# Performance work log

Measured on AMD Instinct MI355X. Metric: run time of the kernel, lower is better.

The kernel has to match this reference:

```python
import jax, jax.numpy as jnp
import numpy as np
import math

DIM, DEPTH, HEADS, DH, MLP = 512, 12, 8, 64, 2048
EPS = 1e-5

def _ln(x, g, b):
    m = jnp.mean(x, -1, keepdims=True)
    v = jnp.var(x, -1, keepdims=True)
    return (x - m) * jax.lax.rsqrt(v + EPS) * g + b

def _gelu(x):
    return jax.nn.gelu(x, approximate=False)  # torch nn.GELU default = exact erf

def _conv1d(x, w, b):
    # x: [B, Cin, T], w: [Cout, Cin, 7], 'same' padding
    y = jax.lax.conv_general_dilated(x, w, (1,), [(3, 3)], dimension_numbers=('NCH', 'OIH', 'NCH'))
    return y + b[None, :, None]

def setup_inputs() -> dict:
    key = jax.random.key(0)
    ks = iter(jax.random.split(key, 64))
    def w(shape, s=0.02):
        return jax.random.normal(next(ks), shape, jnp.float32) * s
    return {
        'x': jax.random.normal(next(ks), (2, 1024), jnp.float32),
        'timesteps': jax.random.uniform(next(ks), (2,), jnp.float32) * 1000.0,
        'cond': jax.random.normal(next(ks), (2, 64, DIM), jnp.float32),
        'conv_w1': w((DIM // 2, 1, 7)), 'conv_b1': jnp.zeros((DIM // 2,), jnp.float32),
        'conv_w2': w((DIM, DIM // 2, 7)), 'conv_b2': jnp.zeros((DIM,), jnp.float32),
        'tpe_w1': w((DIM, 4 * DIM)), 'tpe_b1': jnp.zeros((4 * DIM,), jnp.float32),
        'tpe_w2': w((4 * DIM, DIM)), 'tpe_b2': jnp.zeros((DIM,), jnp.float32),
        'ln1_g': jnp.ones((DEPTH, DIM), jnp.float32), 'ln1_b': jnp.zeros((DEPTH, DIM), jnp.float32),
        'wq': w((DEPTH, DIM, HEADS * DH)), 'wkv': w((DEPTH, DIM, 2 * DH)),
        'wo': w((DEPTH, HEADS * DH, DIM)), 'bo': jnp.zeros((DEPTH, DIM), jnp.float32),
        'ln2_g': jnp.ones((DEPTH, DIM), jnp.float32), 'ln2_b': jnp.zeros((DEPTH, DIM), jnp.float32),
        'ffn_w1': w((DEPTH, DIM, MLP)), 'ffn_b1': jnp.zeros((DEPTH, MLP), jnp.float32),
        'ffn_w2': w((DEPTH, MLP, DIM)), 'ffn_b2': jnp.zeros((DEPTH, DIM), jnp.float32),
        'tm_w1': w((DEPTH, DIM, 4 * DIM)), 'tm_b1': jnp.zeros((DEPTH, 4 * DIM), jnp.float32),
        'tm_w2': w((DEPTH, 4 * DIM, DIM)), 'tm_b2': jnp.zeros((DEPTH, DIM), jnp.float32),
        'fn_g': jnp.ones((DIM,), jnp.float32), 'fn_b': jnp.zeros((DIM,), jnp.float32),
        'out_w1': w((DIM, 2 * DIM)), 'out_b1': jnp.zeros((2 * DIM,), jnp.float32),
        'out_w2': w((2 * DIM, 1)), 'out_b2': jnp.zeros((1,), jnp.float32),
    }

def reference(x, timesteps, cond, conv_w1, conv_b1, conv_w2, conv_b2,
              tpe_w1, tpe_b1, tpe_w2, tpe_b2,
              ln1_g, ln1_b, wq, wkv, wo, bo, ln2_g, ln2_b,
              ffn_w1, ffn_b1, ffn_w2, ffn_b2, tm_w1, tm_b1, tm_w2, tm_b2,
              fn_g, fn_b, out_w1, out_b1, out_w2, out_b2):
    b, T = x.shape
    # audio encoder: conv -> relu -> conv -> relu
    h = _conv1d(x[:, None, :], conv_w1, conv_b1)
    h = jax.nn.relu(h)
    h = _conv1d(h, conv_w2, conv_b2)
    h = jax.nn.relu(h)
    h = h.transpose(0, 2, 1)  # [b, T, dim]
    # sinusoidal time embedding + MLP
    half = DIM // 2
    freqs = jnp.exp(jnp.arange(half, dtype=jnp.float32) * (-math.log(10000.0) / (half - 1)))
    te = timesteps[:, None] * freqs[None, :]
    te = jnp.concatenate([jnp.sin(te), jnp.cos(te)], axis=-1)  # [b, dim]
    time_emb = _gelu(te @ tpe_w1 + tpe_b1) @ tpe_w2 + tpe_b2
    # concat text conditioning tokens
    h = jnp.concatenate([h, cond], axis=1)  # [b, n, dim]
    bsz, n, _ = h.shape
    scale = DH ** -0.5

    def block(hx, p):
        g1, b1, Wq, Wkv, Wo, Bo, g2, b2, F1, Fb1, F2, Fb2, T1, Tb1, T2, Tb2 = p
        tm = _gelu(time_emb @ T1 + Tb1) @ T2 + Tb2  # [b, dim]
        hx = _ln(hx, g1, b1)
        q = (hx @ Wq).reshape(bsz, n, HEADS, DH).transpose(0, 2, 1, 3)  # [b,h,n,d]
        kv = hx @ Wkv
        k, v = kv[..., :DH], kv[..., DH:]  # shared single KV head [b,n,d]
        dots = jnp.einsum('bhnd,bmd->bhnm', q, k) * scale
        attn = jax.nn.softmax(dots, axis=-1)
        o = jnp.einsum('bhnm,bmd->bhnd', attn, v)
        o = o.transpose(0, 2, 1, 3).reshape(bsz, n, HEADS * DH) @ Wo + Bo
        hx = hx + o
        hx = hx + tm[:, None, :]
        hx = _ln(hx, g2, b2)
        hx = hx + (_gelu(hx @ F1 + Fb1) @ F2 + Fb2)
        return hx, None

    h, _ = jax.lax.scan(block, h, (ln1_g, ln1_b, wq, wkv, wo, bo, ln2_g, ln2_b,
                                   ffn_w1, ffn_b1, ffn_w2, ffn_b2,
                                   tm_w1, tm_b1, tm_w2, tm_b2))
    h = _ln(h, fn_g, fn_b)
    h = _gelu(h @ out_w1 + out_b1) @ out_w2 + out_b2  # [b, n, 1]
    return h[:, :T, 0]
```

## Files before the change

### kernel.cpp

```cpp
#include <hip/hip_runtime.h>
#include <hip/hip_bf16.h>
#include <math.h>


typedef unsigned short u16;
typedef __attribute__((ext_vector_type(8))) short short8;
typedef __attribute__((ext_vector_type(8))) unsigned short ushort8;
typedef __attribute__((ext_vector_type(4))) float f32x4;

#define MFMA_B16(a, b, c) __builtin_amdgcn_mfma_f32_16x16x32_bf16(a, b, c, 0, 0, 0)

__device__ __forceinline__ float gelu_f(float x) {
  return 0.5f * x * (1.f + erff(x * 0.70710678118654752f));
}
__device__ __forceinline__ u16 f2b(float x) {
  union { float f; unsigned u; } v;
  v.f = x;
  unsigned r = (v.u + 0x7FFF + ((v.u >> 16) & 1)) >> 16;
  return (u16)r;
}
__device__ __forceinline__ float b2f(u16 u) {
  union { unsigned u; float f; } v;
  v.u = ((unsigned)u) << 16;
  return v.f;
}

#define MODE_BIAS 1
#define MODE_GELU 2
#define MODE_RES 4
#define MODE_TM 8
#define MODE_OUT16 16
#define MODE_KVT 32
#define MODE_RELU 64
#define MODE_CONVROW 128

__global__ void te_k(const float* __restrict__ ts, float* __restrict__ te) {
  int t = threadIdx.x;
  int b = t >> 8, i = t & 255;
  float tv = ts[b];
  float fr = __expf((float)i * (-9.210340371976184f / 255.f));
  float arg = tv * fr;
  te[b * 512 + i] = sinf(arg);
  te[b * 512 + 256 + i] = cosf(arg);
}

__global__ __launch_bounds__(256) void mlpA_k(const float* __restrict__ A,
                                              const float* __restrict__ B,
                                              float* __restrict__ part, int K,
                                              int N, long sA, long sB) {
  int l = blockIdx.z;
  const float* Ap = A + (size_t)l * sA;
  const float* Bp = B + (size_t)l * sB;
  int KS = K >> 7;
  int tid = threadIdx.x;
  int c16 = tid & 15;
  int col = blockIdx.x * 64 + c16 * 4;
  int kr = tid >> 4;
  int k0 = blockIdx.y * 128 + kr;
  float4 a0 = {0.f, 0.f, 0.f, 0.f}, a1 = {0.f, 0.f, 0.f, 0.f};
#pragma unroll
  for (int i = 0; i < 8; ++i) {
    int k = k0 + i * 16;
    float4 bv = *(const float4*)&Bp[(size_t)k * N + col];
    float x0 = Ap[k], x1 = Ap[K + k];
    a0.x = fmaf(x0, bv.x, a0.x);
    a0.y = fmaf(x0, bv.y, a0.y);
    a0.z = fmaf(x0, bv.z, a0.z);
    a0.w = fmaf(x0, bv.w, a0.w);
    a1.x = fmaf(x1, bv.x, a1.x);
    a1.y = fmaf(x1, bv.y, a1.y);
    a1.z = fmaf(x1, bv.z, a1.z);
    a1.w = fmaf(x1, bv.w, a1.w);
  }
#pragma unroll
  for (int off = 16; off < 64; off <<= 1) {
    a0.x += __shfl_xor(a0.x, off);
    a0.y += __shfl_xor(a0.y, off);
    a0.z += __shfl_xor(a0.z, off);
    a0.w += __shfl_xor(a0.w, off);
    a1.x += __shfl_xor(a1.x, off);
    a1.y += __shfl_xor(a1.y, off);
    a1.z += __shfl_xor(a1.z, off);
    a1.w += __shfl_xor(a1.w, off);
  }
  __shared__ float red[4][2][64];
  int w = tid >> 6, lane = tid & 63;
  if (lane < 16) {
    *(float4*)&red[w][0][c16 * 4] = a0;
    *(float4*)&red[w][1][c16 * 4] = a1;
  }
  __syncthreads();
  if (tid < 128) {
    int m = tid >> 6, c = tid & 63;
    float s = red[0][m][c] + red[1][m][c] + red[2][m][c] + red[3][m][c];
    part[(((size_t)l * KS + blockIdx.y) * 2 + m) * N + blockIdx.x * 64 + c] = s;
  }
}

__global__ __launch_bounds__(256) void mlpB_k(const float* __restrict__ part,
                                              const float* __restrict__ bias,
                                              float* __restrict__ C, int N,
                                              int lgN, int KS, int dogelu,
                                              long sb, long sC) {
  int idx = blockIdx.x * 256 + threadIdx.x;
  int col = idx & (N - 1);
  int lm = idx >> lgN;
  int m = lm & 1, l = lm >> 1;
  float s = 0.f;
  for (int ks = 0; ks < KS; ++ks)
    s += part[(((size_t)l * KS + ks) * 2 + m) * N + col];
  s += bias[(size_t)l * sb + col];
  if (dogelu) s = gelu_f(s);
  C[(size_t)l * sC + (size_t)m * N + col] = s;
}

__global__ __launch_bounds__(256) void conv1_k(const float* __restrict__ x,
                                               const float* __restrict__ w1,
                                               const float* __restrict__ b1,
                                               float* __restrict__ buf1) {
  int idx = blockIdx.x * 256 + threadIdx.x;
  int t = idx & 1023, co = (idx >> 10) & 255, b = idx >> 18;
  float acc = b1[co];
#pragma unroll
  for (int k = 0; k < 7; ++k) {
    int gt = t + k - 3;
    if (gt >= 0 && gt < 1024)
      acc = fmaf(w1[co * 7 + k], x[b * 1024 + gt], acc);
  }
  buf1[idx] = fmaxf(acc, 0.f);
}

__global__ __launch_bounds__(256) void im2col_k(const float* __restrict__ buf1,
                                                u16* __restrict__ A16) {
  int idx = blockIdx.x * 256 + threadIdx.x;
  int c = idx % 1792;
  int m = idx / 1792;
  int b = m >> 10, tt = m & 1023;
  int ci = c / 7, k = c - ci * 7;
  int gt = tt + k - 3;
  float v = (gt >= 0 && gt < 1024) ? buf1[((b * 256) + ci) * 1024 + gt] : 0.f;
  A16[idx] = f2b(v);
}

__global__ void cond_k(const float* __restrict__ cond,
                       float* __restrict__ hbuf) {
  int idx = blockIdx.x * 256 + threadIdx.x;
  int b = idx >> 15, rem = idx & 32767;
  int j = rem >> 9, cc = rem & 511;
  hbuf[(size_t)(b * 1088 + 1024 + j) * 512 + cc] = cond[idx];
}

__global__ __launch_bounds__(256) void ln_k(float* __restrict__ h,
                                            u16* __restrict__ h16,
                                            const float* __restrict__ g,
                                            const float* __restrict__ bb) {
  int row = blockIdx.x;
  float* p = h + (size_t)row * 512;
  int t = threadIdx.x;
  float x0 = p[t], x1 = p[t + 256];
  float s = x0 + x1, q = x0 * x0 + x1 * x1;
#pragma unroll
  for (int off = 1; off < 64; off <<= 1) {
    s += __shfl_xor(s, off);
    q += __shfl_xor(q, off);
  }
  __shared__ float ps[4], pq[4];
  int w = t >> 6, lane = t & 63;
  if (lane == 0) {
    ps[w] = s;
    pq[w] = q;
  }
  __syncthreads();
  s = ps[0] + ps[1] + ps[2] + ps[3];
  q = pq[0] + pq[1] + pq[2] + pq[3];
  float mean = s * (1.f / 512.f);
  float var = q * (1.f / 512.f) - mean * mean;
  float rs = rsqrtf(var + 1e-5f);
  float v0 = (x0 - mean) * rs * g[t] + bb[t];
  float v1 = (x1 - mean) * rs * g[t + 256] + bb[t + 256];
  p[t] = v0;
  p[t + 256] = v1;
  h16[(size_t)row * 512 + t] = f2b(v0);
  h16[(size_t)row * 512 + t + 256] = f2b(v1);
}

__device__ __forceinline__ void wcvt_tile(float (*T)[65],
                                          const float* __restrict__ src,
                                          u16* __restrict__ dst, int K, int N,
                                          int tk, int tn, int t) {
  int kl = t >> 2, nseg = (t & 3) * 16;
#pragma unroll
  for (int j = 0; j < 4; ++j) {
    float4 v =
        *(const float4*)&src[(size_t)(tk * 64 + kl) * N + tn * 64 + nseg + j * 4];
    T[nseg + j * 4 + 0][kl] = v.x;
    T[nseg + j * 4 + 1][kl] = v.y;
    T[nseg + j * 4 + 2][kl] = v.z;
    T[nseg + j * 4 + 3][kl] = v.w;
  }
  __syncthreads();
  int nl = t >> 2, kseg = (t & 3) * 16;
#pragma unroll
  for (int j = 0; j < 4; ++j) {
    ushort4 o;
    o.x = f2b(T[nl][kseg + j * 4 + 0]);
    o.y = f2b(T[nl][kseg + j * 4 + 1]);
    o.z = f2b(T[nl][kseg + j * 4 + 2]);
    o.w = f2b(T[nl][kseg + j * 4 + 3]);
    *(ushort4*)&dst[(size_t)(tn * 64 + nl) * K + tk * 64 + kseg + j * 4] = o;
  }
}

__global__ __launch_bounds__(256) void wcvt5_k(
    const float* wq, const float* wkv, const float* wo, const float* w1,
    const float* w2, u16* dq, u16* dkv, u16* dwo, u16* d1, u16* d2) {
  __shared__ float T[64][65];
  int bid = blockIdx.x, t = threadIdx.x;
  if (bid < 64) {
    wcvt_tile(T, wq, dq, 512, 512, bid >> 3, bid & 7, t);
  } else if (bid < 80) {
    int id = bid - 64;
    wcvt_tile(T, wkv, dkv, 512, 128, id >> 1, id & 1, t);
  } else if (bid < 144) {
    int id = bid - 80;
    wcvt_tile(T, wo, dwo, 512, 512, id >> 3, id & 7, t);
  } else if (bid < 400) {
    int id = bid - 144;
    wcvt_tile(T, w1, d1, 512, 2048, id >> 5, id & 31, t);
  } else {
    int id = bid - 400;
    wcvt_tile(T, w2, d2, 2048, 512, id >> 3, id & 7, t);
  }
}

__global__ __launch_bounds__(256) void wcvtT_k(const float* src, u16* dst,
                                               int K, int N) {
  __shared__ float T[64][65];
  int nt = N >> 6;
  int tk = blockIdx.x / nt, tn = blockIdx.x % nt;
  wcvt_tile(T, src, dst, K, N, tk, tn, threadIdx.x);
}

__global__ __launch_bounds__(256) void fcvt_k(const float* __restrict__ src,
                                              u16* __restrict__ dst, int n) {
  int i = (blockIdx.x * 256 + threadIdx.x) * 4;
  if (i >= n) return;
  float4 v = *(const float4*)&src[i];
  ushort4 o;
  o.x = f2b(v.x);
  o.y = f2b(v.y);
  o.z = f2b(v.z);
  o.w = f2b(v.w);
  *(ushort4*)&dst[i] = o;
}

__global__ __launch_bounds__(256) void bgemm2_k(
    const u16* __restrict__ A, const u16* __restrict__ B,
    const float* __restrict__ bias, const float* __restrict__ tmv,
    const float* __restrict__ res, float* __restrict__ Cf,
    u16* __restrict__ C16, u16* __restrict__ C16b, float* __restrict__ part,
    int K, int N, int Kblk, int MN, int mode) {
  __shared__ u16 As[2][64 * 72];
  __shared__ u16 Bs[2][64 * 72];
  int t = threadIdx.x;
  int n0 = blockIdx.x * 64, m0 = blockIdx.y * 64;
  int kz = blockIdx.z;
  int wid = t >> 6, lane = t & 63;
  int quad = lane >> 4, l15 = lane & 15;
  int wr = (wid >> 1) * 32, wc = (wid & 1) * 32;
  int sr = t >> 2, sc = (t & 3) * 16;
  const u16* Ap = A + (size_t)(m0 + sr) * K + (size_t)kz * Kblk + sc;
  const u16* Bp = B + (size_t)(n0 + sr) * K + (size_t)kz * Kblk + sc;

  f32x4 acc[2][2];
#pragma unroll
  for (int i = 0; i < 2; ++i)
#pragma unroll
    for (int j = 0; j < 2; ++j) acc[i][j] = (f32x4){0.f, 0.f, 0.f, 0.f};

  int nt = Kblk >> 6;
  ushort8 ra0 = *(const ushort8*)Ap;
  ushort8 ra1 = *(const ushort8*)(Ap + 8);
  ushort8 rb0 = *(const ushort8*)Bp;
  ushort8 rb1 = *(const ushort8*)(Bp + 8);
  *(ushort8*)&As[0][sr * 72 + sc] = ra0;
  *(ushort8*)&As[0][sr * 72 + sc + 8] = ra1;
  *(ushort8*)&Bs[0][sr * 72 + sc] = rb0;
  *(ushort8*)&Bs[0][sr * 72 + sc + 8] = rb1;
  __syncthreads();
  int cur = 0;
  for (int tt = 0; tt < nt; ++tt) {
    if (tt + 1 < nt) {
      const u16* ap = Ap + (tt + 1) * 64;
      const u16* bp = Bp + (tt + 1) * 64;
      ra0 = *(const ushort8*)ap;
      ra1 = *(const ushort8*)(ap + 8);
      rb0 = *(const ushort8*)bp;
      rb1 = *(const ushort8*)(bp + 8);
    }
    short8 af[2][2], bf[2][2];
#pragma unroll
    for (int s = 0; s < 2; ++s)
#pragma unroll
      for (int i = 0; i < 2; ++i) {
        af[i][s] =
            *(const short8*)&As[cur][(wr + i * 16 + l15) * 72 + s * 32 + quad * 8];
        bf[i][s] =
            *(const short8*)&Bs[cur][(wc + i * 16 + l15) * 72 + s * 32 + quad * 8];
      }
#pragma unroll
    for (int s = 0; s < 2; ++s)
#pragma unroll
      for (int i = 0; i < 2; ++i)
#pragma unroll
        for (int j = 0; j < 2; ++j)
          acc[i][j] = MFMA_B16(af[i][s], bf[j][s], acc[i][j]);
    if (tt + 1 < nt) {
      int nx = cur ^ 1;
      *(ushort8*)&As[nx][sr * 72 + sc] = ra0;
      *(ushort8*)&As[nx][sr * 72 + sc + 8] = ra1;
      *(ushort8*)&Bs[nx][sr * 72 + sc] = rb0;
      *(ushort8*)&Bs[nx][sr * 72 + sc + 8] = rb1;
      __syncthreads();
      cur = nx;
    }
  }

  if (gridDim.z > 1) {
#pragma unroll
    for (int i = 0; i < 2; ++i)
#pragma unroll
      for (int reg = 0; reg < 4; ++reg) {
        int row = m0 + wr + i * 16 + quad * 4 + reg;
#pragma unroll
        for (int j = 0; j < 2; ++j) {
          int col = n0 + wc + j * 16 + l15;
          part[(size_t)kz * MN + (size_t)row * N + col] = acc[i][j][reg];
        }
      }
    return;
  }

#pragma unroll
  for (int i = 0; i < 2; ++i) {
#pragma unroll
    for (int reg = 0; reg < 4; ++reg) {
      int row = m0 + wr + i * 16 + quad * 4 + reg;
      int orow = (mode & MODE_CONVROW) ? row + ((row >> 10) << 6) : row;
#pragma unroll
      for (int j = 0; j < 2; ++j) {
        int col = n0 + wc + j * 16 + l15;
        float v = acc[i][j][reg];
        if (mode & MODE_BIAS) v += bias[col];
        if (mode & MODE_TM) v += tmv[(row >= 1088 ? 512 : 0) + col];
        if (mode & MODE_RES) v += res[(size_t)orow * 512 + col];
        if (mode & MODE_GELU) v = gelu_f(v);
        if (mode & MODE_RELU) v = fmaxf(v, 0.f);
        if (mode & MODE_KVT) {
          if (col < 64)
            C16[orow * 64 + col] = f2b(v);
          else
            C16b[(size_t)(col - 64) * 2176 + orow] = f2b(v);
        } else if (mode & MODE_OUT16) {
          C16[(size_t)orow * N + col] = f2b(v);
        } else {
          Cf[(size_t)orow * N + col] = v;
        }
      }
    }
  }
}

__global__ __launch_bounds__(256) void bred_k(
    const float* __restrict__ part, const float* __restrict__ bias,
    const float* __restrict__ tmv, const float* __restrict__ res,
    float* __restrict__ Cf, u16* __restrict__ C16, u16* __restrict__ C16b,
    int MN, int Nmask, int lgN, int S, int mode) {
  int idx = (blockIdx.x * 256 + threadIdx.x) * 4;
  if (idx >= MN) return;
  int row = idx >> lgN;
  int col = idx & Nmask;
  float4 s = *(const float4*)&part[idx];
  for (int ss = 1; ss < S; ++ss) {
    float4 p = *(const float4*)&part[(size_t)ss * MN + idx];
    s.x += p.x;
    s.y += p.y;
    s.z += p.z;
    s.w += p.w;
  }
  float v[4] = {s.x, s.y, s.z, s.w};
#pragma unroll
  for (int j = 0; j < 4; ++j) {
    float vv = v[j];
    int c = col + j;
    if (mode & MODE_BIAS) vv += bias[c];
    if (mode & MODE_TM) vv += tmv[(row >= 1088 ? 512 : 0) + c];
    if (mode & MODE_RES) vv += res[(size_t)row * 512 + c];
    if (mode & MODE_GELU) vv = gelu_f(vv);
    v[j] = vv;
  }
  if (mode & MODE_KVT) {
    if (col < 64) {
      ushort4 o;
      o.x = f2b(v[0]);
      o.y = f2b(v[1]);
      o.z = f2b(v[2]);
      o.w = f2b(v[3]);
      *(ushort4*)&C16[row * 64 + col] = o;
    } else {
#pragma unroll
      for (int j = 0; j < 4; ++j)
        C16b[(size_t)(col - 64 + j) * 2176 + row] = f2b(v[j]);
    }
  } else if (mode & MODE_OUT16) {
    ushort4 o;
    o.x = f2b(v[0]);
    o.y = f2b(v[1]);
    o.z = f2b(v[2]);
    o.w = f2b(v[3]);
    *(ushort4*)&C16[idx] = o;
  } else {
    float4 o = {v[0], v[1], v[2], v[3]};
    *(float4*)&Cf[idx] = o;
  }
}

__global__ __launch_bounds__(256) void attn_k(const u16* __restrict__ q,
                                              const u16* __restrict__ k16,
                                              const u16* __restrict__ vT16,
                                              u16* __restrict__ o) {
  __shared__ u16 Qs[64 * 72];
  __shared__ u16 Ks[64 * 72];
  __shared__ u16 VT[64 * 72];
  __shared__ u16 Ps[64 * 72];
  int t = threadIdx.x;
  int qt = blockIdx.x, h = blockIdx.y, b = blockIdx.z;
  int wid = t >> 6, lane = t & 63;
  int quad = lane >> 4, l15 = lane & 15;
  int w16 = wid * 16;
  {
    int r = t >> 2, seg = (t & 3) * 16;
    const u16* qp = q + (size_t)(b * 1088 + qt * 64 + r) * 512 + h * 64 + seg;
    *(ushort8*)&Qs[r * 72 + seg] = *(const ushort8*)qp;
    *(ushort8*)&Qs[r * 72 + seg + 8] = *(const ushort8*)(qp + 8);
  }
  f32x4 accO[4];
#pragma unroll
  for (int i = 0; i < 4; ++i) accO[i] = (f32x4){0.f, 0.f, 0.f, 0.f};
  float mi[4] = {-1e30f, -1e30f, -1e30f, -1e30f};
  float li[4] = {0.f, 0.f, 0.f, 0.f};

  for (int kt = 0; kt < 17; ++kt) {
    __syncthreads();
    {
      int r = t >> 2, seg = (t & 3) * 16;
      const u16* kp = k16 + (size_t)(b * 1088 + kt * 64 + r) * 64 + seg;
      *(ushort8*)&Ks[r * 72 + seg] = *(const ushort8*)kp;
      *(ushort8*)&Ks[r * 72 + seg + 8] = *(const ushort8*)(kp + 8);
      const u16* vp = vT16 + (size_t)r * 2176 + b * 1088 + kt * 64 + seg;
      *(ushort8*)&VT[r * 72 + seg] = *(const ushort8*)vp;
      *(ushort8*)&VT[r * 72 + seg + 8] = *(const ushort8*)(vp + 8);
    }
    __syncthreads();
    f32x4 sc[4];
#pragma unroll
    for (int sn = 0; sn < 4; ++sn) sc[sn] = (f32x4){0.f, 0.f, 0.f, 0.f};
#pragma unroll
    for (int s = 0; s < 2; ++s) {
      short8 a = *(const short8*)&Qs[(w16 + l15) * 72 + s * 32 + quad * 8];
#pragma unroll
      for (int sn = 0; sn < 4; ++sn) {
        short8 bb = *(const short8*)&Ks[(sn * 16 + l15) * 72 + s * 32 + quad * 8];
        sc[sn] = MFMA_B16(a, bb, sc[sn]);
      }
    }
#pragma unroll
    for (int reg = 0; reg < 4; ++reg) {
      float s0 = sc[0][reg] * 0.125f, s1 = sc[1][reg] * 0.125f;
      float s2 = sc[2][reg] * 0.125f, s3 = sc[3][reg] * 0.125f;
      float mx = fmaxf(fmaxf(s0, s1), fmaxf(s2, s3));
#pragma unroll
      for (int off = 1; off < 16; off <<= 1) mx = fmaxf(mx, __shfl_xor(mx, off));
      float mn = fmaxf(mi[reg], mx);
      float al = __expf(mi[reg] - mn);
      mi[reg] = mn;
      float p0 = __expf(s0 - mn), p1 = __expf(s1 - mn);
      float p2 = __expf(s2 - mn), p3 = __expf(s3 - mn);
      int rr = (w16 + quad * 4 + reg) * 72 + l15;
      Ps[rr] = f2b(p0);
      Ps[rr + 16] = f2b(p1);
      Ps[rr + 32] = f2b(p2);
      Ps[rr + 48] = f2b(p3);
      float psum = p0 + p1 + p2 + p3;
#pragma unroll
      for (int off = 1; off < 16; off <<= 1) psum += __shfl_xor(psum, off);
      li[reg] = li[reg] * al + psum;
#pragma unroll
      for (int sn = 0; sn < 4; ++sn) accO[sn][reg] *= al;
    }
#pragma unroll
    for (int s = 0; s < 2; ++s) {
      short8 pa = *(const short8*)&Ps[(w16 + l15) * 72 + s * 32 + quad * 8];
#pragma unroll
      for (int sn = 0; sn < 4; ++sn) {
        short8 vb = *(const short8*)&VT[(sn * 16 + l15) * 72 + s * 32 + quad * 8];
        accO[sn] = MFMA_B16(pa, vb, accO[sn]);
      }
    }
  }
#pragma unroll
  for (int reg = 0; reg < 4; ++reg) {
    float inv = 1.f / li[reg];
    int row = b * 1088 + qt * 64 + w16 + quad * 4 + reg;
#pragma unroll
    for (int sn = 0; sn < 4; ++sn) {
      o[(size_t)row * 512 + h * 64 + sn * 16 + l15] = f2b(accO[sn][reg] * inv);
    }
  }
}

__global__ __launch_bounds__(256) void outvec_k(const u16* __restrict__ G,
                                               const float* __restrict__ w,
                                               const float* __restrict__ b2,
                                               float* __restrict__ out) {
  int row = blockIdx.x;
  int b = row >> 10, tt = row & 1023;
  const u16* g = G + (size_t)(b * 1088 + tt) * 1024;
  int k0 = threadIdx.x * 4;
  ushort4 gv = *(const ushort4*)&g[k0];
  float acc = b2f(gv.x) * w[k0] + b2f(gv.y) * w[k0 + 1] +
              b2f(gv.z) * w[k0 + 2] + b2f(gv.w) * w[k0 + 3];
#pragma unroll
  for (int off = 1; off < 64; off <<= 1) acc += __shfl_xor(acc, off);
  __shared__ float part[4];
  int wv = threadIdx.x >> 6, lane = threadIdx.x & 63;
  if (lane == 0) part[wv] = acc;
  __syncthreads();
  if (threadIdx.x == 0) {
    out[row] = part[0] + part[1] + part[2] + part[3] + b2[0];
  }
}

extern "C" void kernel_launch(void* const* d_in, const int* in_sizes, int n_in,
                              void* d_out, int out_size, void* d_ws,
                              size_t ws_size, hipStream_t stream) {
  (void)in_sizes;
  (void)n_in;
  (void)out_size;
  const float* x = (const float*)d_in[0];
  const float* timesteps = (const float*)d_in[1];
  const float* cond = (const float*)d_in[2];
  const float* conv_w1 = (const float*)d_in[3];
  const float* conv_b1 = (const float*)d_in[4];
  const float* conv_w2 = (const float*)d_in[5];
  const float* conv_b2 = (const float*)d_in[6];
  const float* tpe_w1 = (const float*)d_in[7];
  const float* tpe_b1 = (const float*)d_in[8];
  const float* tpe_w2 = (const float*)d_in[9];
  const float* tpe_b2 = (const float*)d_in[10];
  const float* ln1_g = (const float*)d_in[11];
  const float* ln1_b = (const float*)d_in[12];
  const float* wq = (const float*)d_in[13];
  const float* wkv = (const float*)d_in[14];
  const float* wo = (const float*)d_in[15];
  const float* bo = (const float*)d_in[16];
  const float* ln2_g = (const float*)d_in[17];
  const float* ln2_b = (const float*)d_in[18];
  const float* ffn_w1 = (const float*)d_in[19];
  const float* ffn_b1 = (const float*)d_in[20];
  const float* ffn_w2 = (const float*)d_in[21];
  const float* ffn_b2 = (const float*)d_in[22];
  const float* tm_w1 = (const float*)d_in[23];
  const float* tm_b1 = (const float*)d_in[24];
  const float* tm_w2 = (const float*)d_in[25];
  const float* tm_b2 = (const float*)d_in[26];
  const float* fn_g = (const float*)d_in[27];
  const float* fn_b = (const float*)d_in[28];
  const float* out_w1 = (const float*)d_in[29];
  const float* out_b1 = (const float*)d_in[30];
  const float* out_w2 = (const float*)d_in[31];
  const float* out_b2 = (const float*)d_in[32];

  float* w = (float*)d_ws;
  float* te = w + 0;
  float* tpe_mid = w + 1024;
  float* time_emb = w + 5120;
  float* tm_mid = w + 6144;
  float* tm = w + 55296;
  float* hbuf = w + 131072;
  u16* q16 = (u16*)(w + 1245184);
  float* buf1 = w + 1245184;
  u16* hb16 = (u16*)(w + 1802240);
  u16* k16 = (u16*)(w + 2359296);
  u16* vT16 = (u16*)(w + 2428928);
  u16* mid16 = (u16*)(w + 2498560);
  u16* im16 = mid16;
  u16* g16 = mid16;
  u16* wbuf = (u16*)(w + 4726784);
  u16* wq16 = wbuf;
  u16* wkv16 = wbuf + 262144;
  u16* wo16 = wbuf + 327680;
  u16* w116 = wbuf + 589824;
  u16* w216 = wbuf + 1638400;
  u16* cw216 = wbuf;
  u16* ow116 = wbuf;
  float* pmlp = hbuf;
  float* pmid = w + 2498560;
  int big = ws_size >= (size_t)(6070272 + 2228224) * 4 ? 1 : 0;
  float* part2 = w + 6070272;

  te_k<<<1, 512, 0, stream>>>(timesteps, te);
  mlpA_k<<<dim3(32, 4, 1), 256, 0, stream>>>(te, tpe_w1, pmlp, 512, 2048, 0, 0);
  mlpB_k<<<16, 256, 0, stream>>>(pmlp, tpe_b1, tpe_mid, 2048, 11, 4, 1, 0, 0);
  mlpA_k<<<dim3(8, 16, 1), 256, 0, stream>>>(tpe_mid, tpe_w2, pmlp, 2048, 512,
                                             0, 0);
  mlpB_k<<<4, 256, 0, stream>>>(pmlp, tpe_b2, time_emb, 512, 9, 16, 0, 0, 0);
  mlpA_k<<<dim3(32, 4, 12), 256, 0, stream>>>(time_emb, tm_w1, pmlp, 512, 2048,
                                              0, 512L * 2048);
  mlpB_k<<<192, 256, 0, stream>>>(pmlp, tm_b1, tm_mid, 2048, 11, 4, 1, 2048,
                                  2L * 2048);
  mlpA_k<<<dim3(8, 16, 12), 256, 0, stream>>>(tm_mid, tm_w2, pmlp, 2048, 512,
                                              2L * 2048, 2048L * 512);
  mlpB_k<<<48, 256, 0, stream>>>(pmlp, tm_b2, tm, 512, 9, 16, 0, 512,
                                 2L * 512);

  conv1_k<<<2048, 256, 0, stream>>>(x, conv_w1, conv_b1, buf1);
  fcvt_k<<<896, 256, 0, stream>>>(conv_w2, cw216, 917504);
  im2col_k<<<14336, 256, 0, stream>>>(buf1, im16);
  bgemm2_k<<<dim3(8, 32, 1), 256, 0, stream>>>(
      im16, cw216, conv_b2, nullptr, nullptr, hbuf, nullptr, nullptr, nullptr,
      1792, 512, 1792, 0, MODE_BIAS | MODE_RELU | MODE_CONVROW);
  cond_k<<<256, 256, 0, stream>>>(cond, hbuf);

  for (int l = 0; l < 12; ++l) {
    wcvt5_k<<<656, 256, 0, stream>>>(
        wq + (size_t)l * 512 * 512, wkv + (size_t)l * 512 * 128,
        wo + (size_t)l * 512 * 512, ffn_w1 + (size_t)l * 512 * 2048,
        ffn_w2 + (size_t)l * 2048 * 512, wq16, wkv16, wo16, w116, w216);
    ln_k<<<2176, 256, 0, stream>>>(hbuf, hb16, ln1_g + l * 512,
                                   ln1_b + l * 512);
    bgemm2_k<<<dim3(8, 34, 2), 256, 0, stream>>>(
        hb16, wq16, nullptr, nullptr, nullptr, nullptr, nullptr, nullptr,
        pmid, 512, 512, 256, 1114112, 0);
    bred_k<<<1088, 256, 0, stream>>>(pmid, nullptr, nullptr, nullptr, nullptr,
                                     q16, nullptr, 1114112, 511, 9, 2,
                                     MODE_OUT16);
    bgemm2_k<<<dim3(2, 34, 2), 256, 0, stream>>>(
        hb16, wkv16, nullptr, nullptr, nullptr, nullptr, nullptr, nullptr,
        pmid, 512, 128, 256, 278528, 0);
    bred_k<<<272, 256, 0, stream>>>(pmid, nullptr, nullptr, nullptr, nullptr,
                                    k16, vT16, 278528, 127, 7, 2, MODE_KVT);
    attn_k<<<dim3(17, 8, 2), 256, 0, stream>>>(q16, k16, vT16, q16);
    bgemm2_k<<<dim3(8, 34, 2), 256, 0, stream>>>(
        q16, wo16, nullptr, nullptr, nullptr, nullptr, nullptr, nullptr, pmid,
        512, 512, 256, 1114112, 0);
    bred_k<<<1088, 256, 0, stream>>>(pmid, bo + l * 512, tm + l * 1024, hbuf,
                                     hbuf, nullptr, nullptr, 1114112, 511, 9,
                                     2, MODE_BIAS | MODE_TM | MODE_RES);
    ln_k<<<2176, 256, 0, stream>>>(hbuf, hb16, ln2_g + l * 512,
                                   ln2_b + l * 512);
    bgemm2_k<<<dim3(32, 34, 1), 256, 0, stream>>>(
        hb16, w116, ffn_b1 + l * 2048, nullptr, nullptr, nullptr, mid16,
        nullptr, nullptr, 512, 2048, 512, 0,
        MODE_BIAS | MODE_GELU | MODE_OUT16);
    if (big) {
      bgemm2_k<<<dim3(8, 34, 2), 256, 0, stream>>>(
          mid16, w216, nullptr, nullptr, nullptr, nullptr, nullptr, nullptr,
          part2, 2048, 512, 1024, 1114112, 0);
      bred_k<<<1088, 256, 0, stream>>>(part2, ffn_b2 + l * 512, nullptr, hbuf,
                                       hbuf, nullptr, nullptr, 1114112, 511, 9,
                                       2, MODE_BIAS | MODE_RES);
    } else {
      bgemm2_k<<<dim3(8, 34, 1), 256, 0, stream>>>(
          mid16, w216, ffn_b2 + l * 512, nullptr, hbuf, hbuf, nullptr,
          nullptr, nullptr, 2048, 512, 2048, 0, MODE_BIAS | MODE_RES);
    }
  }
  ln_k<<<2176, 256, 0, stream>>>(hbuf, hb16, fn_g, fn_b);
  wcvtT_k<<<128, 256, 0, stream>>>(out_w1, ow116, 512, 1024);
  bgemm2_k<<<dim3(16, 34, 1), 256, 0, stream>>>(
      hb16, ow116, out_b1, nullptr, nullptr, nullptr, g16, nullptr, nullptr,
      512, 1024, 512, 0, MODE_BIAS | MODE_GELU | MODE_OUT16);
  outvec_k<<<2048, 256, 0, stream>>>(g16, out_w2, out_b2, (float*)d_out);
}
```

Baseline: 1.986 ms.

## Split attention over KV halves with double-buffered K/V and merge kernel

Attention is now split across two KV ranges (9 and 8 tiles), doubling the grid from 272 to 544 blocks to better fill the GPU. A separate merge kernel combines the two partial outputs using the saved row max and sum values. The K/V tile loads are also double-buffered through registers, so the next tile's global load overlaps the current tile's MFMA work with one barrier per iteration. This costs an extra kernel launch, partial-output traffic through the workspace, and a bf16 rounding of the partial outputs before the merge.

```diff
diff --git a/kernel.cpp b/kernel.cpp
--- a/kernel.cpp
+++ b/kernel.cpp
@@ -425,52 +425,64 @@
   }
 }
 
-__global__ __launch_bounds__(256) void attn_k(const u16* __restrict__ q,
-                                              const u16* __restrict__ k16,
-                                              const u16* __restrict__ vT16,
-                                              u16* __restrict__ o) {
+__global__ __launch_bounds__(256) void attn2_k(const u16* __restrict__ q,
+                                               const u16* __restrict__ k16,
+                                               const u16* __restrict__ vT16,
+                                               u16* __restrict__ opart,
+                                               float* __restrict__ ml) {
   __shared__ u16 Qs[64 * 72];
-  __shared__ u16 Ks[64 * 72];
-  __shared__ u16 VT[64 * 72];
+  __shared__ u16 Ks[2][64 * 72];
+  __shared__ u16 VT[2][64 * 72];
   __shared__ u16 Ps[64 * 72];
   int t = threadIdx.x;
-  int qt = blockIdx.x, h = blockIdx.y, b = blockIdx.z;
+  int qt = blockIdx.x, h = blockIdx.y;
+  int b = blockIdx.z >> 1, s = blockIdx.z & 1;
+  int kt0 = s * 9;
+  int ktn = 9 - s;
   int wid = t >> 6, lane = t & 63;
   int quad = lane >> 4, l15 = lane & 15;
   int w16 = wid * 16;
+  int r = t >> 2, seg = (t & 3) * 16;
   {
-    int r = t >> 2, seg = (t & 3) * 16;
     const u16* qp = q + (size_t)(b * 1088 + qt * 64 + r) * 512 + h * 64 + seg;
     *(ushort8*)&Qs[r * 72 + seg] = *(const ushort8*)qp;
     *(ushort8*)&Qs[r * 72 + seg + 8] = *(const ushort8*)(qp + 8);
   }
+  const u16* kbase = k16 + (size_t)(b * 1088 + kt0 * 64 + r) * 64 + seg;
+  const u16* vbase = vT16 + (size_t)r * 2176 + b * 1088 + kt0 * 64 + seg;
+  *(ushort8*)&Ks[0][r * 72 + seg] = *(const ushort8*)kbase;
+  *(ushort8*)&Ks[0][r * 72 + seg + 8] = *(const ushort8*)(kbase + 8);
+  *(ushort8*)&VT[0][r * 72 + seg] = *(const ushort8*)vbase;
+  *(ushort8*)&VT[0][r * 72 + seg + 8] = *(const ushort8*)(vbase + 8);
+  __syncthreads();
+
   f32x4 accO[4];
 #pragma unroll
   for (int i = 0; i < 4; ++i) accO[i] = (f32x4){0.f, 0.f, 0.f, 0.f};
   float mi[4] = {-1e30f, -1e30f, -1e30f, -1e30f};
   float li[4] = {0.f, 0.f, 0.f, 0.f};
 
-  for (int kt = 0; kt < 17; ++kt) {
-    __syncthreads();
-    {
-      int r = t >> 2, seg = (t & 3) * 16;
-      const u16* kp = k16 + (size_t)(b * 1088 + kt * 64 + r) * 64 + seg;
-      *(ushort8*)&Ks[r * 72 + seg] = *(const ushort8*)kp;
-      *(ushort8*)&Ks[r * 72 + seg + 8] = *(const ushort8*)(kp + 8);
-      const u16* vp = vT16 + (size_t)r * 2176 + b * 1088 + kt * 64 + seg;
-      *(ushort8*)&VT[r * 72 + seg] = *(const ushort8*)vp;
-      *(ushort8*)&VT[r * 72 + seg + 8] = *(const ushort8*)(vp + 8);
-    }
-    __syncthreads();
+  int cur = 0;
+  ushort8 rk0, rk1, rv0, rv1;
+  for (int kt = 0; kt < ktn; ++kt) {
+    if (kt + 1 < ktn) {
+      const u16* kp = kbase + (size_t)(kt + 1) * 64 * 64;
+      const u16* vp = vbase + (kt + 1) * 64;
+      rk0 = *(const ushort8*)kp;
+      rk1 = *(const ushort8*)(kp + 8);
+      rv0 = *(const ushort8*)vp;
+      rv1 = *(const ushort8*)(vp + 8);
+    }
     f32x4 sc[4];
 #pragma unroll
     for (int sn = 0; sn < 4; ++sn) sc[sn] = (f32x4){0.f, 0.f, 0.f, 0.f};
 #pragma unroll
-    for (int s = 0; s < 2; ++s) {
-      short8 a = *(const short8*)&Qs[(w16 + l15) * 72 + s * 32 + quad * 8];
+    for (int ss = 0; ss < 2; ++ss) {
+      short8 a = *(const short8*)&Qs[(w16 + l15) * 72 + ss * 32 + quad * 8];
 #pragma unroll
       for (int sn = 0; sn < 4; ++sn) {
-        short8 bb = *(const short8*)&Ks[(sn * 16 + l15) * 72 + s * 32 + quad * 8];
+        short8 bb =
+            *(const short8*)&Ks[cur][(sn * 16 + l15) * 72 + ss * 32 + quad * 8];
         sc[sn] = MFMA_B16(a, bb, sc[sn]);
       }
     }
@@ -499,24 +511,67 @@
       for (int sn = 0; sn < 4; ++sn) accO[sn][reg] *= al;
     }
 #pragma unroll
-    for (int s = 0; s < 2; ++s) {
-      short8 pa = *(const short8*)&Ps[(w16 + l15) * 72 + s * 32 + quad * 8];
+    for (int ss = 0; ss < 2; ++ss) {
+      short8 pa = *(const short8*)&Ps[(w16 + l15) * 72 + ss * 32 + quad * 8];
 #pragma unroll
       for (int sn = 0; sn < 4; ++sn) {
-        short8 vb = *(const short8*)&VT[(sn * 16 + l15) * 72 + s * 32 + quad * 8];
+        short8 vb =
+            *(const short8*)&VT[cur][(sn * 16 + l15) * 72 + ss * 32 + quad * 8];
         accO[sn] = MFMA_B16(pa, vb, accO[sn]);
       }
     }
-  }
+    if (kt + 1 < ktn) {
+      int nx = cur ^ 1;
+      *(ushort8*)&Ks[nx][r * 72 + seg] = rk0;
+      *(ushort8*)&Ks[nx][r * 72 + seg + 8] = rk1;
+      *(ushort8*)&VT[nx][r * 72 + seg] = rv0;
+      *(ushort8*)&VT[nx][r * 72 + seg + 8] = rv1;
+      __syncthreads();
+      cur = nx;
+    }
+  }
+  size_t pbase = (((size_t)(s * 2 + b) * 8 + h) * 1088 + qt * 64);
 #pragma unroll
   for (int reg = 0; reg < 4; ++reg) {
     float inv = 1.f / li[reg];
-    int row = b * 1088 + qt * 64 + w16 + quad * 4 + reg;
+    int rr = w16 + quad * 4 + reg;
 #pragma unroll
     for (int sn = 0; sn < 4; ++sn) {
-      o[(size_t)row * 512 + h * 64 + sn * 16 + l15] = f2b(accO[sn][reg] * inv);
-    }
-  }
+      opart[(pbase + rr) * 64 + sn * 16 + l15] = f2b(accO[sn][reg] * inv);
+    }
+    if (l15 == 0) {
+      ml[(pbase + rr) * 2] = mi[reg];
+      ml[(pbase + rr) * 2 + 1] = li[reg];
+    }
+  }
+}
+
+__global__ __launch_bounds__(256) void amerge_k(const u16* __restrict__ opart,
+                                                const float* __restrict__ ml,
+                                                u16* __restrict__ o) {
+  int idx = blockIdx.x * 256 + threadIdx.x;
+  int d4 = (idx & 15) * 4;
+  int rem = idx >> 4;
+  int row = rem % 1088;
+  int bh = rem / 1088;
+  int h = bh & 7, b = bh >> 3;
+  size_t r0 = ((size_t)(0 + b) * 8 + h) * 1088 + row;
+  size_t r1 = ((size_t)(2 + b) * 8 + h) * 1088 + row;
+  float m0 = ml[r0 * 2], l0 = ml[r0 * 2 + 1];
+  float m1 = ml[r1 * 2], l1 = ml[r1 * 2 + 1];
+  float m = fmaxf(m0, m1);
+  float w0 = l0 * __expf(m0 - m), w1 = l1 * __expf(m1 - m);
+  float inv = 1.f / (w0 + w1);
+  w0 *= inv;
+  w1 *= inv;
+  ushort4 a = *(const ushort4*)&opart[r0 * 64 + d4];
+  ushort4 c = *(const ushort4*)&opart[r1 * 64 + d4];
+  ushort4 ov;
+  ov.x = f2b(w0 * b2f(a.x) + w1 * b2f(c.x));
+  ov.y = f2b(w0 * b2f(a.y) + w1 * b2f(c.y));
+  ov.z = f2b(w0 * b2f(a.z) + w1 * b2f(c.z));
+  ov.w = f2b(w0 * b2f(a.w) + w1 * b2f(c.w));
+  *(ushort4*)&o[(size_t)(b * 1088 + row) * 512 + h * 64 + d4] = ov;
 }
 
 __global__ __launch_bounds__(256) void outvec_k(const u16* __restrict__ G,
@@ -606,6 +661,8 @@
   u16* ow116 = wbuf;
   float* pmlp = hbuf;
   float* pmid = w + 2498560;
+  u16* opart16 = (u16*)(w + 2498560);
+  float* aml = w + 2498560 + 1114112;
   int big = ws_size >= (size_t)(6070272 + 2228224) * 4 ? 1 : 0;
   float* part2 = w + 6070272;
 
@@ -650,7 +707,8 @@
         pmid, 512, 128, 256, 278528, 0);
     bred_k<<<272, 256, 0, stream>>>(pmid, nullptr, nullptr, nullptr, nullptr,
                                     k16, vT16, 278528, 127, 7, 2, MODE_KVT);
-    attn_k<<<dim3(17, 8, 2), 256, 0, stream>>>(q16, k16, vT16, q16);
+    attn2_k<<<dim3(17, 8, 4), 256, 0, stream>>>(q16, k16, vT16, opart16, aml);
+    amerge_k<<<1088, 256, 0, stream>>>(opart16, aml, q16);
     bgemm2_k<<<dim3(8, 34, 2), 256, 0, stream>>>(
         q16, wo16, nullptr, nullptr, nullptr, nullptr, nullptr, nullptr, pmid,
         512, 512, 256, 1114112, 0);
```

Result: faster. 1.860 ms (-6.3%).
